# Kernel tuning notes

Measured on AMD Instinct MI355X. Metric: run time of the kernel, lower is better.

The kernel has to match this reference:

```python
import jax, jax.numpy as jnp
import numpy as np

K_PROPOSALS = 16  # Marsaglia-Tsang acceptance rate > 0.95 for alpha > 1/3; P(all 16 rejected) < 1e-20

B, D_IN, H, L = 32768, 1024, 512, 64


def _glorot(key, shape):
    fan_in, fan_out = shape
    return jax.random.normal(key, shape, jnp.float32) * jnp.sqrt(2.0 / (fan_in + fan_out))


def setup_inputs() -> dict:
    key = jax.random.key(0)
    ks = jax.random.split(key, 4)
    return {
        "x": jax.random.normal(ks[0], (B, D_IN), jnp.float32),
        "W0": _glorot(ks[1], (D_IN, H)),
        "b0": jnp.zeros((H,), jnp.float32),
        "W1": _glorot(ks[2], (H, H)),
        "b1": jnp.zeros((H,), jnp.float32),
        "Wl": _glorot(ks[3], (H, L)),
        "bl": jnp.zeros((L,), jnp.float32),
    }


def _marsaglia_tsang_sample(alpha):
    """Vectorized Marsaglia-Tsang gamma(alpha, 1) rejection sampler.
    Draws K_PROPOSALS candidates per element and selects the first accepted one
    (equivalent to the original per-element while-loop, flattened for SIMD)."""
    d = alpha - 1.0 / 3.0                     # [B, L]
    c = 1.0 / jnp.sqrt(9.0 * d)               # [B, L]
    kz, ku = jax.random.split(jax.random.key(1))
    z = jax.random.normal(kz, (K_PROPOSALS,) + alpha.shape, alpha.dtype)   # [K, B, L]
    u = jax.random.uniform(ku, (K_PROPOSALS,) + alpha.shape, alpha.dtype,
                           minval=1e-7, maxval=1.0)                        # [K, B, L]
    v = (1.0 + c * z) ** 3                    # [K, B, L]
    pos = v > 0.0                             # equivalent to z > -1/c (= b1)
    safe_v = jnp.where(pos, v, 1.0)
    # accept iff z > b1 AND log(u) <= b2 (negation of the resampling condition)
    b2 = 0.5 * jnp.square(z) + d - d * safe_v + d * jnp.log(safe_v)
    accept = pos & (jnp.log(u) < b2)          # [K, B, L]
    first = jnp.argmax(accept, axis=0)        # index of first accepted proposal
    samples = d * safe_v                      # [K, B, L]
    return jnp.take_along_axis(samples, first[None], axis=0)[0]  # [B, L]


def reference(x, W0, b0, W1, b1, Wl, bl):
    # dense encoder: two ReLU hidden layers + linear latent head producing alpha
    h = jax.nn.relu(x @ W0 + b0)
    h = jax.nn.relu(h @ W1 + b1)
    # softplus + 0.5 keeps alpha > 1/3 so d > 0 (required by Marsaglia-Tsang)
    alpha = jax.nn.softplus(h @ Wl + bl) + 0.5
    sample = _marsaglia_tsang_sample(alpha)
    return alpha, sample
```

## Files before the change

kernel.cpp:

```cpp
#include <hip/hip_runtime.h>
#include <cstdint>
#include <cstddef>

typedef __attribute__((ext_vector_type(8))) short short8;
typedef __attribute__((ext_vector_type(4))) float floatx4;

constexpr int MDIM = 32768;
constexpr int DIN  = 1024;
constexpr int HDIM = 512;
constexpr int LDIM = 64;
constexpr uint32_t BL = (uint32_t)MDIM * (uint32_t)LDIM;

__host__ __device__ __forceinline__ void tf2x32(uint32_t k0, uint32_t k1,
                                                uint32_t x0, uint32_t x1,
                                                uint32_t& o0, uint32_t& o1) {
  const uint32_t k2 = k0 ^ k1 ^ 0x1BD11BDAu;
  x0 += k0; x1 += k1;
#define TFR(r) { x0 += x1; x1 = (x1 << (r)) | (x1 >> (32 - (r))); x1 ^= x0; }
  TFR(13) TFR(15) TFR(26) TFR(6)
  x0 += k1; x1 += k2 + 1u;
  TFR(17) TFR(29) TFR(16) TFR(24)
  x0 += k2; x1 += k0 + 2u;
  TFR(13) TFR(15) TFR(26) TFR(6)
  x0 += k0; x1 += k1 + 3u;
  TFR(17) TFR(29) TFR(16) TFR(24)
  x0 += k1; x1 += k2 + 4u;
  TFR(13) TFR(15) TFR(26) TFR(6)
  x0 += k2; x1 += k0 + 5u;
#undef TFR
  o0 = x0; o1 = x1;
}

__device__ __forceinline__ uint32_t tf_bits(uint32_t k0, uint32_t k1, uint32_t j) {
  uint32_t o0, o1;
  tf2x32(k0, k1, 0u, j, o0, o1);
  return o0 ^ o1;
}

__device__ __forceinline__ float b2f(unsigned short s) {
  return __uint_as_float((uint32_t)s << 16);
}
__device__ __forceinline__ unsigned short f2b(float f) {
  uint32_t u = __float_as_uint(f);
  u += 0x7fffu + ((u >> 16) & 1u);
  return (unsigned short)(u >> 16);
}
__device__ __forceinline__ void split3(float x, unsigned short& h,
                                       unsigned short& l, unsigned short& l2) {
  h = f2b(x);
  const float r = __fsub_rn(x, b2f(h));
  l = f2b(r);
  const float r2 = __fsub_rn(r, b2f(l));
  l2 = f2b(r2);
}

__device__ __forceinline__ float erfinv_f32(float x) {
  const float xx = __fmul_rn(x, x);
  float w = -log1pf(-xx);
  float p;
  if (w < 5.0f) {
    w = __fadd_rn(w, -2.5f);
    p = 2.81022636e-08f;
    p = __fadd_rn(__fmul_rn(p, w), 3.43273939e-07f);
    p = __fadd_rn(__fmul_rn(p, w), -3.5233877e-06f);
    p = __fadd_rn(__fmul_rn(p, w), -4.39150654e-06f);
    p = __fadd_rn(__fmul_rn(p, w), 0.00021858087f);
    p = __fadd_rn(__fmul_rn(p, w), -0.00125372503f);
    p = __fadd_rn(__fmul_rn(p, w), -0.00417768164f);
    p = __fadd_rn(__fmul_rn(p, w), 0.246640727f);
    p = __fadd_rn(__fmul_rn(p, w), 1.50140941f);
  } else {
    w = __fadd_rn(sqrtf(w), -3.0f);
    p = -0.000200214257f;
    p = __fadd_rn(__fmul_rn(p, w), 0.000100950558f);
    p = __fadd_rn(__fmul_rn(p, w), 0.00134934322f);
    p = __fadd_rn(__fmul_rn(p, w), -0.00367342844f);
    p = __fadd_rn(__fmul_rn(p, w), 0.00573950773f);
    p = __fadd_rn(__fmul_rn(p, w), -0.0076224613f);
    p = __fadd_rn(__fmul_rn(p, w), 0.00943887047f);
    p = __fadd_rn(__fmul_rn(p, w), 1.00167406f);
    p = __fadd_rn(__fmul_rn(p, w), 2.83297682f);
  }
  return __fmul_rn(p, x);
}

#define LO_N  (-0x1.fffffep-1f)
#define DIFF_N (2.0f)
#define SQRT2_F ((float)1.4142135623730951)
#define DIFF_U (0x1.fffffcp-1f)
#define MINV_U (1e-7f)
#define THIRD_F ((float)(1.0 / 3.0))

__device__ float gamma_sample(float alpha, uint32_t e,
                              uint32_t kz0, uint32_t kz1,
                              uint32_t ku0, uint32_t ku1) {
  const float d = __fsub_rn(alpha, THIRD_F);
  const float c = __fdiv_rn(1.0f, sqrtf(__fmul_rn(9.0f, d)));
  float samp0 = 0.0f;
#pragma unroll 1
  for (int k = 0; k < 16; ++k) {
    const uint32_t j = (uint32_t)k * BL + e;
    const uint32_t zb = tf_bits(kz0, kz1, j);
    const uint32_t ub = tf_bits(ku0, ku1, j);
    const float fz = __fsub_rn(__uint_as_float((zb >> 9) | 0x3f800000u), 1.0f);
    float un = __fadd_rn(__fmul_rn(fz, DIFF_N), LO_N);
    un = fmaxf(un, LO_N);
    const float z = __fmul_rn(SQRT2_F, erfinv_f32(un));
    const float fu = __fsub_rn(__uint_as_float((ub >> 9) | 0x3f800000u), 1.0f);
    float uu = __fadd_rn(__fmul_rn(fu, DIFF_U), MINV_U);
    uu = fmaxf(uu, MINV_U);
    const float t1 = __fadd_rn(1.0f, __fmul_rn(c, z));
    const float v = __fmul_rn(t1, __fmul_rn(t1, t1));
    const bool pos = (v > 0.0f);
    const float sv = pos ? v : 1.0f;
    const float b2 = __fadd_rn(
        __fsub_rn(__fadd_rn(__fmul_rn(0.5f, __fmul_rn(z, z)), d),
                  __fmul_rn(d, sv)),
        __fmul_rn(d, logf(sv)));
    const float lu = logf(uu);
    const float s = __fmul_rn(d, sv);
    if (k == 0) samp0 = s;
    if (pos && (lu < b2)) return s;
  }
  return samp0;
}

__global__ __launch_bounds__(256) void split_transpose(
    const float* __restrict__ W, unsigned short* __restrict__ D, int K, int N) {
  __shared__ unsigned short th[32][33], tl[32][33], tl2[32][33];
  const int t = threadIdx.x;
  const int nb = N / 32;
  const int k0 = (blockIdx.x / nb) * 32, n0 = (blockIdx.x % nb) * 32;
#pragma unroll
  for (int i = 0; i < 4; ++i) {
    const int e = i * 256 + t;
    const int kk = e >> 5, nn = e & 31;
    const float x = W[(size_t)(k0 + kk) * N + (n0 + nn)];
    split3(x, th[kk][nn], tl[kk][nn], tl2[kk][nn]);
  }
  __syncthreads();
  const size_t PL = (size_t)N * K;
#pragma unroll
  for (int i = 0; i < 4; ++i) {
    const int e = i * 256 + t;
    const int nn = e >> 5, kk = e & 31;
    const size_t o = (size_t)(n0 + nn) * K + (k0 + kk);
    D[o] = th[kk][nn];
    D[PL + o] = tl[kk][nn];
    D[2 * PL + o] = tl2[kk][nn];
  }
}

template <int K>
__global__ __launch_bounds__(256) void gemm_split_mfma(
    const float* __restrict__ A, const unsigned short* __restrict__ BT,
    const float* __restrict__ bias, float* __restrict__ C) {
  constexpr int N = 512;
  constexpr size_t PL = (size_t)N * K;
  __shared__ unsigned short As[3][128 * 32];
  __shared__ unsigned short Bs[3][128 * 32];
  const int t = threadIdx.x;
  const int lane = t & 63, w = t >> 6;
  const int wm = w >> 1, wn = w & 1;
  const int ln = lane & 15, kq = lane >> 4;
  const int bm = blockIdx.y * 128, bn = blockIdx.x * 128;

  floatx4 acc[4][4];
#pragma unroll
  for (int i = 0; i < 4; ++i)
#pragma unroll
    for (int j = 0; j < 4; ++j) acc[i][j] = (floatx4)0.0f;

  for (int k0 = 0; k0 < K; k0 += 32) {
#pragma unroll
    for (int p = 0; p < 3; ++p)
#pragma unroll
      for (int i = 0; i < 2; ++i) {
        const int e = w * 1024 + i * 512 + lane * 8;
        const int n = e >> 5, kc = e & 31;
        const unsigned short* g = BT + p * PL + (size_t)(bn + n) * K + (k0 + kc);
        __builtin_amdgcn_global_load_lds(
            (const __attribute__((address_space(1))) unsigned int*)g,
            (__attribute__((address_space(3))) unsigned int*)&Bs[p][w * 1024 + i * 512],
            16, 0, 0);
      }
#pragma unroll
    for (int it = 0; it < 4; ++it) {
      const int e4 = (it * 256 + t) * 4;
      const int m = e4 >> 5, kc = e4 & 31;
      const float4 q = *reinterpret_cast<const float4*>(
          &A[(size_t)(bm + m) * K + (k0 + kc)]);
      ushort4 h, l, l2;
      split3(q.x, h.x, l.x, l2.x);
      split3(q.y, h.y, l.y, l2.y);
      split3(q.z, h.z, l.z, l2.z);
      split3(q.w, h.w, l.w, l2.w);
      *reinterpret_cast<ushort4*>(&As[0][m * 32 + kc]) = h;
      *reinterpret_cast<ushort4*>(&As[1][m * 32 + kc]) = l;
      *reinterpret_cast<ushort4*>(&As[2][m * 32 + kc]) = l2;
    }
    __syncthreads();
    short8 af[3][4], bf[3][4];
#pragma unroll
    for (int mi = 0; mi < 4; ++mi)
#pragma unroll
      for (int p = 0; p < 3; ++p)
        af[p][mi] = *reinterpret_cast<const short8*>(
            &As[p][(wm * 64 + mi * 16 + ln) * 32 + kq * 8]);
#pragma unroll
    for (int ni = 0; ni < 4; ++ni)
#pragma unroll
      for (int p = 0; p < 3; ++p)
        bf[p][ni] = *reinterpret_cast<const short8*>(
            &Bs[p][(wn * 64 + ni * 16 + ln) * 32 + kq * 8]);
#pragma unroll
    for (int mi = 0; mi < 4; ++mi)
#pragma unroll
      for (int ni = 0; ni < 4; ++ni) {
        floatx4 a = acc[mi][ni];
        a = __builtin_amdgcn_mfma_f32_16x16x32_bf16(af[0][mi], bf[0][ni], a, 0, 0, 0);
        a = __builtin_amdgcn_mfma_f32_16x16x32_bf16(af[0][mi], bf[1][ni], a, 0, 0, 0);
        a = __builtin_amdgcn_mfma_f32_16x16x32_bf16(af[1][mi], bf[0][ni], a, 0, 0, 0);
        a = __builtin_amdgcn_mfma_f32_16x16x32_bf16(af[1][mi], bf[1][ni], a, 0, 0, 0);
        a = __builtin_amdgcn_mfma_f32_16x16x32_bf16(af[0][mi], bf[2][ni], a, 0, 0, 0);
        a = __builtin_amdgcn_mfma_f32_16x16x32_bf16(af[2][mi], bf[0][ni], a, 0, 0, 0);
        acc[mi][ni] = a;
      }
    __syncthreads();
  }
#pragma unroll
  for (int ni = 0; ni < 4; ++ni) {
    const int n = bn + wn * 64 + ni * 16 + ln;
    const float bb = bias[n];
#pragma unroll
    for (int mi = 0; mi < 4; ++mi)
#pragma unroll
      for (int r = 0; r < 4; ++r) {
        const int m = bm + wm * 64 + mi * 16 + kq * 4 + r;
        C[(size_t)m * N + n] = fmaxf(__fadd_rn(acc[mi][ni][r], bb), 0.0f);
      }
  }
}

__global__ __launch_bounds__(256) void gemm3_sampler(
    const float* __restrict__ A, const float* __restrict__ Wl,
    const float* __restrict__ bl, float* __restrict__ out,
    uint32_t kz0, uint32_t kz1, uint32_t ku0, uint32_t ku1) {
  constexpr int BM = 64, BK = 16, K = 512, N = 64;
  constexpr int LDA = BM + 4, LDB = N + 4;
  __shared__ float Ash[BK * LDA];
  __shared__ float Bsh[BK * LDB];
  const int t = threadIdx.x;
  const int tx = t % 16, ty = t / 16;
  const int bm = blockIdx.x * BM;
  float acc[4][4] = {};
  const int aRow = t / 4, aCol = (t % 4) * 4;
  const int bRow = t / 16, bCol = (t % 16) * 4;

  for (int k0 = 0; k0 < K; k0 += BK) {
    {
      const float4 q = *reinterpret_cast<const float4*>(
          A + (size_t)(bm + aRow) * K + (k0 + aCol));
      Ash[(aCol + 0) * LDA + aRow] = q.x;
      Ash[(aCol + 1) * LDA + aRow] = q.y;
      Ash[(aCol + 2) * LDA + aRow] = q.z;
      Ash[(aCol + 3) * LDA + aRow] = q.w;
    }
    {
      const float4 q = *reinterpret_cast<const float4*>(
          Wl + (size_t)(k0 + bRow) * N + bCol);
      *reinterpret_cast<float4*>(&Bsh[bRow * LDB + bCol]) = q;
    }
    __syncthreads();
#pragma unroll
    for (int k = 0; k < BK; ++k) {
      float a[4], b[4];
#pragma unroll
      for (int i = 0; i < 4; ++i) a[i] = Ash[k * LDA + ty * 4 + i];
#pragma unroll
      for (int j = 0; j < 4; ++j) b[j] = Bsh[k * LDB + tx * 4 + j];
#pragma unroll
      for (int i = 0; i < 4; ++i)
#pragma unroll
        for (int j = 0; j < 4; ++j) acc[i][j] = fmaf(a[i], b[j], acc[i][j]);
    }
    __syncthreads();
  }

  float bv[4];
#pragma unroll
  for (int j = 0; j < 4; ++j) bv[j] = bl[tx * 4 + j];

  for (int i = 0; i < 4; ++i) {
    const int row = bm + ty * 4 + i;
    float av[4], sv4[4];
    for (int j = 0; j < 4; ++j) {
      const float x = __fadd_rn(acc[i][j], bv[j]);
      const float sp = __fadd_rn(fmaxf(x, 0.0f), log1pf(expf(-fabsf(x))));
      const float alpha = __fadd_rn(sp, 0.5f);
      const uint32_t e = (uint32_t)row * 64u + (uint32_t)(tx * 4 + j);
      const float s = gamma_sample(alpha, e, kz0, kz1, ku0, ku1);
      av[j] = alpha;
      sv4[j] = s;
    }
    *reinterpret_cast<float4*>(&out[(size_t)row * 64 + tx * 4]) =
        *reinterpret_cast<float4*>(av);
    *reinterpret_cast<float4*>(&out[(size_t)BL + (size_t)row * 64 + tx * 4]) =
        *reinterpret_cast<float4*>(sv4);
  }
}

extern "C" void kernel_launch(void* const* d_in, const int* in_sizes, int n_in,
                              void* d_out, int out_size, void* d_ws, size_t ws_size,
                              hipStream_t stream) {
  (void)in_sizes; (void)n_in; (void)out_size; (void)ws_size;
  const float* x  = (const float*)d_in[0];
  const float* W0 = (const float*)d_in[1];
  const float* b0 = (const float*)d_in[2];
  const float* W1 = (const float*)d_in[3];
  const float* b1 = (const float*)d_in[4];
  const float* Wl = (const float*)d_in[5];
  const float* bl = (const float*)d_in[6];
  float* h1 = (float*)d_ws;
  float* h2 = h1 + (size_t)MDIM * HDIM;
  float* out = (float*)d_out;

  unsigned short* W0T = (unsigned short*)out;
  unsigned short* W1T = (unsigned short*)(out + BL);

  uint32_t kz0, kz1, ku0, ku1;
  tf2x32(0u, 1u, 0u, 0u, kz0, kz1);
  tf2x32(0u, 1u, 0u, 1u, ku0, ku1);

  split_transpose<<<dim3((DIN / 32) * (HDIM / 32)), 256, 0, stream>>>(
      W0, W0T, DIN, HDIM);
  split_transpose<<<dim3((HDIM / 32) * (HDIM / 32)), 256, 0, stream>>>(
      W1, W1T, HDIM, HDIM);

  dim3 g12(HDIM / 128, MDIM / 128);
  gemm_split_mfma<DIN><<<g12, 256, 0, stream>>>(x, W0T, b0, h1);
  gemm_split_mfma<HDIM><<<g12, 256, 0, stream>>>(h1, W1T, b1, h2);
  gemm3_sampler<<<dim3(MDIM / 64), 256, 0, stream>>>(h2, Wl, bl, out,
                                                     kz0, kz1, ku0, ku1);
}
```

Before: 521.4 us.

## Swizzle LDS layout in split GEMMs and move latent head to MFMA

The two big split-bf16 MFMA GEMMs now store A and B tiles in LDS with an XOR swizzle on the 8-element k-chunk index, which is meant to cut LDS bank conflicts on the fragment reads. The third GEMM (512->64 latent head) is rewritten from scalar FP32 FMAs to the same three-way bf16 split MFMA scheme. Its weight is split and transposed into the workspace after h1 is consumed. The output stores become scalar and strided instead of float4 vectors, and the split-bf16 emulation may differ slightly from the FP32 result.

```diff
diff --git a/kernel.cpp b/kernel.cpp
--- a/kernel.cpp
+++ b/kernel.cpp
@@ -164,6 +164,8 @@
   const int wm = w >> 1, wn = w & 1;
   const int ln = lane & 15, kq = lane >> 4;
   const int bm = blockIdx.y * 128, bn = blockIdx.x * 128;
+  const int rq = kq ^ ((ln >> 1) & 3);
+  const int kcs = ((lane & 3) ^ ((lane >> 3) & 3)) * 8;
 
   floatx4 acc[4][4];
 #pragma unroll
@@ -177,8 +179,8 @@
 #pragma unroll
       for (int i = 0; i < 2; ++i) {
         const int e = w * 1024 + i * 512 + lane * 8;
-        const int n = e >> 5, kc = e & 31;
-        const unsigned short* g = BT + p * PL + (size_t)(bn + n) * K + (k0 + kc);
+        const int n = e >> 5;
+        const unsigned short* g = BT + p * PL + (size_t)(bn + n) * K + (k0 + kcs);
         __builtin_amdgcn_global_load_lds(
             (const __attribute__((address_space(1))) unsigned int*)g,
             (__attribute__((address_space(3))) unsigned int*)&Bs[p][w * 1024 + i * 512],
@@ -195,9 +197,10 @@
       split3(q.y, h.y, l.y, l2.y);
       split3(q.z, h.z, l.z, l2.z);
       split3(q.w, h.w, l.w, l2.w);
-      *reinterpret_cast<ushort4*>(&As[0][m * 32 + kc]) = h;
-      *reinterpret_cast<ushort4*>(&As[1][m * 32 + kc]) = l;
-      *reinterpret_cast<ushort4*>(&As[2][m * 32 + kc]) = l2;
+      const int si = m * 32 + (((kc >> 3) ^ ((m >> 1) & 3)) << 3) + (kc & 7);
+      *reinterpret_cast<ushort4*>(&As[0][si]) = h;
+      *reinterpret_cast<ushort4*>(&As[1][si]) = l;
+      *reinterpret_cast<ushort4*>(&As[2][si]) = l2;
     }
     __syncthreads();
     short8 af[3][4], bf[3][4];
@@ -206,13 +209,13 @@
 #pragma unroll
       for (int p = 0; p < 3; ++p)
         af[p][mi] = *reinterpret_cast<const short8*>(
-            &As[p][(wm * 64 + mi * 16 + ln) * 32 + kq * 8]);
+            &As[p][(wm * 64 + mi * 16 + ln) * 32 + rq * 8]);
 #pragma unroll
     for (int ni = 0; ni < 4; ++ni)
 #pragma unroll
       for (int p = 0; p < 3; ++p)
         bf[p][ni] = *reinterpret_cast<const short8*>(
-            &Bs[p][(wn * 64 + ni * 16 + ln) * 32 + kq * 8]);
+            &Bs[p][(wn * 64 + ni * 16 + ln) * 32 + rq * 8]);
 #pragma unroll
     for (int mi = 0; mi < 4; ++mi)
 #pragma unroll
@@ -243,70 +246,90 @@
 }
 
 __global__ __launch_bounds__(256) void gemm3_sampler(
-    const float* __restrict__ A, const float* __restrict__ Wl,
+    const float* __restrict__ A, const unsigned short* __restrict__ BT,
     const float* __restrict__ bl, float* __restrict__ out,
     uint32_t kz0, uint32_t kz1, uint32_t ku0, uint32_t ku1) {
-  constexpr int BM = 64, BK = 16, K = 512, N = 64;
-  constexpr int LDA = BM + 4, LDB = N + 4;
-  __shared__ float Ash[BK * LDA];
-  __shared__ float Bsh[BK * LDB];
+  constexpr int K = 512, N = 64;
+  constexpr size_t PL = (size_t)N * K;
+  __shared__ unsigned short As[3][64 * 32];
+  __shared__ unsigned short Bs[3][64 * 32];
   const int t = threadIdx.x;
-  const int tx = t % 16, ty = t / 16;
-  const int bm = blockIdx.x * BM;
-  float acc[4][4] = {};
-  const int aRow = t / 4, aCol = (t % 4) * 4;
-  const int bRow = t / 16, bCol = (t % 16) * 4;
-
-  for (int k0 = 0; k0 < K; k0 += BK) {
-    {
+  const int lane = t & 63, w = t >> 6;
+  const int ln = lane & 15, kq = lane >> 4;
+  const int bm = blockIdx.x * 64;
+  const int rq = kq ^ ((ln >> 1) & 3);
+  const int kcs = ((lane & 3) ^ ((lane >> 3) & 3)) * 8;
+
+  floatx4 acc[4];
+#pragma unroll
+  for (int j = 0; j < 4; ++j) acc[j] = (floatx4)0.0f;
+
+  for (int k0 = 0; k0 < K; k0 += 32) {
+#pragma unroll
+    for (int p = 0; p < 3; ++p) {
+      const int n = w * 16 + (lane >> 2);
+      const unsigned short* g = BT + p * PL + (size_t)n * K + (k0 + kcs);
+      __builtin_amdgcn_global_load_lds(
+          (const __attribute__((address_space(1))) unsigned int*)g,
+          (__attribute__((address_space(3))) unsigned int*)&Bs[p][w * 512],
+          16, 0, 0);
+    }
+#pragma unroll
+    for (int it = 0; it < 2; ++it) {
+      const int e4 = (it * 256 + t) * 4;
+      const int m = e4 >> 5, kc = e4 & 31;
       const float4 q = *reinterpret_cast<const float4*>(
-          A + (size_t)(bm + aRow) * K + (k0 + aCol));
-      Ash[(aCol + 0) * LDA + aRow] = q.x;
-      Ash[(aCol + 1) * LDA + aRow] = q.y;
-      Ash[(aCol + 2) * LDA + aRow] = q.z;
-      Ash[(aCol + 3) * LDA + aRow] = q.w;
-    }
-    {
-      const float4 q = *reinterpret_cast<const float4*>(
-          Wl + (size_t)(k0 + bRow) * N + bCol);
-      *reinterpret_cast<float4*>(&Bsh[bRow * LDB + bCol]) = q;
+          &A[(size_t)(bm + m) * K + (k0 + kc)]);
+      ushort4 h, l, l2;
+      split3(q.x, h.x, l.x, l2.x);
+      split3(q.y, h.y, l.y, l2.y);
+      split3(q.z, h.z, l.z, l2.z);
+      split3(q.w, h.w, l.w, l2.w);
+      const int si = m * 32 + (((kc >> 3) ^ ((m >> 1) & 3)) << 3) + (kc & 7);
+      *reinterpret_cast<ushort4*>(&As[0][si]) = h;
+      *reinterpret_cast<ushort4*>(&As[1][si]) = l;
+      *reinterpret_cast<ushort4*>(&As[2][si]) = l2;
     }
     __syncthreads();
-#pragma unroll
-    for (int k = 0; k < BK; ++k) {
-      float a[4], b[4];
-#pragma unroll
-      for (int i = 0; i < 4; ++i) a[i] = Ash[k * LDA + ty * 4 + i];
-#pragma unroll
-      for (int j = 0; j < 4; ++j) b[j] = Bsh[k * LDB + tx * 4 + j];
-#pragma unroll
-      for (int i = 0; i < 4; ++i)
-#pragma unroll
-        for (int j = 0; j < 4; ++j) acc[i][j] = fmaf(a[i], b[j], acc[i][j]);
+    short8 af[3];
+#pragma unroll
+    for (int p = 0; p < 3; ++p)
+      af[p] = *reinterpret_cast<const short8*>(
+          &As[p][(w * 16 + ln) * 32 + rq * 8]);
+#pragma unroll
+    for (int ni = 0; ni < 4; ++ni) {
+      const short8 b0 = *reinterpret_cast<const short8*>(
+          &Bs[0][(ni * 16 + ln) * 32 + rq * 8]);
+      const short8 b1 = *reinterpret_cast<const short8*>(
+          &Bs[1][(ni * 16 + ln) * 32 + rq * 8]);
+      const short8 b2 = *reinterpret_cast<const short8*>(
+          &Bs[2][(ni * 16 + ln) * 32 + rq * 8]);
+      floatx4 a = acc[ni];
+      a = __builtin_amdgcn_mfma_f32_16x16x32_bf16(af[0], b0, a, 0, 0, 0);
+      a = __builtin_amdgcn_mfma_f32_16x16x32_bf16(af[0], b1, a, 0, 0, 0);
+      a = __builtin_amdgcn_mfma_f32_16x16x32_bf16(af[1], b0, a, 0, 0, 0);
+      a = __builtin_amdgcn_mfma_f32_16x16x32_bf16(af[1], b1, a, 0, 0, 0);
+      a = __builtin_amdgcn_mfma_f32_16x16x32_bf16(af[0], b2, a, 0, 0, 0);
+      a = __builtin_amdgcn_mfma_f32_16x16x32_bf16(af[2], b0, a, 0, 0, 0);
+      acc[ni] = a;
     }
     __syncthreads();
   }
-
-  float bv[4];
-#pragma unroll
-  for (int j = 0; j < 4; ++j) bv[j] = bl[tx * 4 + j];
-
-  for (int i = 0; i < 4; ++i) {
-    const int row = bm + ty * 4 + i;
-    float av[4], sv4[4];
-    for (int j = 0; j < 4; ++j) {
-      const float x = __fadd_rn(acc[i][j], bv[j]);
+#pragma unroll
+  for (int ni = 0; ni < 4; ++ni) {
+    const int n = ni * 16 + ln;
+    const float bb = bl[n];
+#pragma unroll
+    for (int r = 0; r < 4; ++r) {
+      const int m = bm + w * 16 + kq * 4 + r;
+      const float x = __fadd_rn(acc[ni][r], bb);
       const float sp = __fadd_rn(fmaxf(x, 0.0f), log1pf(expf(-fabsf(x))));
       const float alpha = __fadd_rn(sp, 0.5f);
-      const uint32_t e = (uint32_t)row * 64u + (uint32_t)(tx * 4 + j);
+      const uint32_t e = (uint32_t)m * 64u + (uint32_t)n;
       const float s = gamma_sample(alpha, e, kz0, kz1, ku0, ku1);
-      av[j] = alpha;
-      sv4[j] = s;
-    }
-    *reinterpret_cast<float4*>(&out[(size_t)row * 64 + tx * 4]) =
-        *reinterpret_cast<float4*>(av);
-    *reinterpret_cast<float4*>(&out[(size_t)BL + (size_t)row * 64 + tx * 4]) =
-        *reinterpret_cast<float4*>(sv4);
+      out[(size_t)m * 64 + n] = alpha;
+      out[(size_t)BL + (size_t)m * 64 + n] = s;
+    }
   }
 }
 
@@ -327,6 +350,7 @@
 
   unsigned short* W0T = (unsigned short*)out;
   unsigned short* W1T = (unsigned short*)(out + BL);
+  unsigned short* WlT = (unsigned short*)d_ws;
 
   uint32_t kz0, kz1, ku0, ku1;
   tf2x32(0u, 1u, 0u, 0u, kz0, kz1);
@@ -340,6 +364,10 @@
   dim3 g12(HDIM / 128, MDIM / 128);
   gemm_split_mfma<DIN><<<g12, 256, 0, stream>>>(x, W0T, b0, h1);
   gemm_split_mfma<HDIM><<<g12, 256, 0, stream>>>(h1, W1T, b1, h2);
-  gemm3_sampler<<<dim3(MDIM / 64), 256, 0, stream>>>(h2, Wl, bl, out,
+
+  split_transpose<<<dim3((HDIM / 32) * (LDIM / 32)), 256, 0, stream>>>(
+      Wl, WlT, HDIM, LDIM);
+
+  gemm3_sampler<<<dim3(MDIM / 64), 256, 0, stream>>>(h2, WlT, bl, out,
                                                      kz0, kz1, ku0, ku1);
 }
```

Result: faster. 502.2 us (-3.7%).
